# Optimization experiments

Measured on AMD Instinct MI355X. Metric: run time of the kernel, lower is better.

The kernel has to match this reference:

```python
import jax, jax.numpy as jnp
import numpy as np


def setup_inputs() -> dict:
    key = jax.random.key(0)
    ks = jax.random.split(key, 6)
    T, n_vars, n_channels, hidden = 2048, 64, 256, 512
    # VarianceScaling(2.0,'fan_in','uniform') ~ uniform(-limit, limit), limit=sqrt(3*2/fan_in)
    limit = float(np.sqrt(3.0 * 2.0 / n_channels))
    return {
        "enriched_history": jax.random.normal(ks[0], (T, n_vars, n_channels), dtype=jnp.float32),
        "target_mask": jax.random.randint(ks[1], (n_vars,), 0, 2, dtype=jnp.int32),
        "intervention_mask": jax.random.randint(ks[2], (n_vars,), 0, 2, dtype=jnp.int32),
        "W_target": jax.random.uniform(ks[3], (n_channels, hidden), jnp.float32, -limit, limit),
        "b_target": jnp.zeros((hidden,), jnp.float32),
        "W_intervention": jax.random.uniform(ks[4], (n_channels, hidden), jnp.float32, -limit, limit),
        "b_intervention": jnp.zeros((hidden,), jnp.float32),
        "W_other": jax.random.uniform(ks[5], (n_channels, hidden), jnp.float32, -limit, limit),
        "b_other": jnp.zeros((hidden,), jnp.float32),
    }


def reference(enriched_history, target_mask, intervention_mask,
              W_target, b_target, W_intervention, b_intervention,
              W_other, b_other):
    T, n_vars, n_channels = enriched_history.shape
    tm = target_mask.astype(jnp.float32)                       # [n_vars]
    im = intervention_mask.astype(jnp.float32) * (1.0 - tm)    # exclusivity
    om = (1.0 - tm) * (1.0 - im)

    flat = enriched_history.reshape(T * n_vars, n_channels)    # [T*n_vars, C]
    proj_t = flat @ W_target + b_target                        # [T*n_vars, H]
    proj_i = flat @ W_intervention + b_intervention
    proj_o = flat @ W_other + b_other

    # Faithful to original: jnp.repeat(mask, T) -> each variable's flag repeated T times
    tm_flat = jnp.repeat(tm, T)
    im_flat = jnp.repeat(im, T)
    om_flat = jnp.repeat(om, T)

    combined = (proj_t * tm_flat[:, None]
                + proj_i * im_flat[:, None]
                + proj_o * om_flat[:, None])
    return combined.reshape(T, n_vars, -1)
```

## Files before the change

### kernel.cpp

```cpp
#include <hip/hip_runtime.h>

typedef float f32x4 __attribute__((ext_vector_type(4)));
typedef unsigned short u16x8 __attribute__((ext_vector_type(8)));
typedef __bf16 bf16x8 __attribute__((ext_vector_type(8)));

__global__ __launch_bounds__(256) void convert_w_kernel(
    const float* __restrict__ Wt_, const float* __restrict__ Wi_,
    const float* __restrict__ Wo_, unsigned short* __restrict__ out)
{
    __shared__ unsigned short tile[64][72];

    const int b    = blockIdx.x;
    const int role = b >> 5;
    const int kt   = (b & 31) >> 3;
    const int nt   = b & 7;
    const float* __restrict__ W = (role == 0) ? Wt_ : ((role == 1) ? Wi_ : Wo_);

    const int t  = threadIdx.x;
    const int r0 = t >> 4;
    const int c4 = (t & 15) << 2;

#pragma unroll
    for (int j = 0; j < 4; ++j) {
        const int kl = r0 + j * 16;
        f32x4 v = *(const f32x4*)(W + (size_t)(kt * 64 + kl) * 512 + nt * 64 + c4);
#pragma unroll
        for (int e = 0; e < 4; ++e)
            tile[c4 + e][kl] = __builtin_bit_cast(unsigned short, (__bf16)v[e]);
    }
    __syncthreads();

    const int cs = t & 7;
#pragma unroll
    for (int p = 0; p < 2; ++p) {
        const int r = (t >> 3) + p * 32;
        u16x8 v = *(const u16x8*)&tile[r][cs * 8];
        *(u16x8*)(out + (size_t)role * 512 * 256 +
                  (size_t)(nt * 64 + r) * 256 + kt * 64 + cs * 8) = v;
    }
}

__global__ __launch_bounds__(512, 3) void role_proj_kernel(
    const float* __restrict__ A,
    const int* __restrict__ tmask,
    const int* __restrict__ imask,
    const unsigned short* __restrict__ Wws,
    const float* __restrict__ bt, const float* __restrict__ bi,
    const float* __restrict__ bo,
    float* __restrict__ C)
{
    __shared__ unsigned short As[64 * 256];

    const int tid = threadIdx.x;
    const int m0  = blockIdx.x * 64;

    const int mi   = blockIdx.x >> 5;
    const int role = tmask[mi] ? 0 : (imask[mi] ? 1 : 2);
    const unsigned short* __restrict__ W = Wws + (size_t)role * (512 * 256);
    const float* __restrict__ bias = (role == 0) ? bt : ((role == 1) ? bi : bo);

    f32x4 ld[4][2];
#pragma unroll
    for (int j = 0; j < 4; ++j) {
        const int u   = tid + 512 * j;
        const int row = u >> 5;
        const int sl  = u & 31;
        const f32x4* src = (const f32x4*)(A + (size_t)(m0 + row) * 256 + sl * 8);
        ld[j][0] = __builtin_nontemporal_load(src);
        ld[j][1] = __builtin_nontemporal_load(src + 1);
    }
#pragma unroll
    for (int j = 0; j < 4; ++j) {
        const int u   = tid + 512 * j;
        const int row = u >> 5;
        const int sl  = u & 31;
        bf16x8 pk;
        pk[0] = (__bf16)ld[j][0][0]; pk[1] = (__bf16)ld[j][0][1];
        pk[2] = (__bf16)ld[j][0][2]; pk[3] = (__bf16)ld[j][0][3];
        pk[4] = (__bf16)ld[j][1][0]; pk[5] = (__bf16)ld[j][1][1];
        pk[6] = (__bf16)ld[j][1][2]; pk[7] = (__bf16)ld[j][1][3];
        *(bf16x8*)&As[row * 256 + ((sl ^ (row & 7)) << 3)] = pk;
    }
    __syncthreads();

    const int lane  = tid & 63;
    const int wid   = tid >> 6;
    const int l15   = lane & 15;
    const int l4    = lane >> 4;
    const int nbase = wid * 64;
    const int r7    = l15 & 7;

#pragma unroll
    for (int fn = 0; fn < 4; ++fn) {
        const unsigned short* wp =
            W + (size_t)(nbase + fn * 16 + l15) * 256 + l4 * 8;

        f32x4 acc[4] = {};

#pragma unroll 1
        for (int ks = 0; ks < 8; ++ks) {
            const u16x8 bfr = *(const u16x8*)(wp + ks * 32);
            u16x8 afr[4];
#pragma unroll
            for (int fm = 0; fm < 4; ++fm) {
                const int row  = fm * 16 + l15;
                const int slot = (ks * 4 + l4) ^ r7;
                afr[fm] = *(const u16x8*)&As[row * 256 + slot * 8];
            }
#pragma unroll
            for (int fm = 0; fm < 4; ++fm) {
                acc[fm] = __builtin_amdgcn_mfma_f32_16x16x32_bf16(
                    __builtin_bit_cast(bf16x8, bfr),
                    __builtin_bit_cast(bf16x8, afr[fm]),
                    acc[fm], 0, 0, 0);
            }
        }

        const int col = nbase + fn * 16 + l4 * 4;
        const f32x4 bv = *(const f32x4*)(bias + col);
#pragma unroll
        for (int fm = 0; fm < 4; ++fm) {
            const int row = m0 + fm * 16 + l15;
            *(f32x4*)(C + (size_t)row * 512 + col) = acc[fm] + bv;
        }
    }
}

extern "C" void kernel_launch(void* const* d_in, const int* in_sizes, int n_in,
                              void* d_out, int out_size, void* d_ws, size_t ws_size,
                              hipStream_t stream) {
    const float* A   = (const float*)d_in[0];
    const int*   tm  = (const int*)d_in[1];
    const int*   im  = (const int*)d_in[2];
    const float* Wt_ = (const float*)d_in[3];
    const float* bt  = (const float*)d_in[4];
    const float* Wi_ = (const float*)d_in[5];
    const float* bi  = (const float*)d_in[6];
    const float* Wo_ = (const float*)d_in[7];
    const float* bo  = (const float*)d_in[8];

    unsigned short* Wws = (unsigned short*)d_ws;

    hipLaunchKernelGGL(convert_w_kernel, dim3(96), dim3(256),
                       0, stream, Wt_, Wi_, Wo_, Wws);

    hipLaunchKernelGGL(role_proj_kernel, dim3(2048), dim3(512),
                       0, stream, A, tm, im, Wws, bt, bi, bo, (float*)d_out);
}
```

Baseline: 137.4 us.

## Keep A fragments in registers per wave and drop LDS staging

The GEMM kernel no longer stages the A tile in shared memory. Each wave now loads its own 32 rows directly from global memory, converts them to bf16 and keeps them in registers, then loops over all 512 output columns, streaming W fragments from global or L2. This removes LDS writes and reads and the block barrier, and switches to 256-thread blocks with a smaller grid. In exchange each wave reads far more W per MFMA (the whole of W per 32 rows instead of per 64 rows), register pressure rises, and A loads become strided by row instead of fully coalesced.

```diff
diff --git a/kernel.cpp b/kernel.cpp
--- a/kernel.cpp
+++ b/kernel.cpp
@@ -40,7 +40,7 @@
     }
 }
 
-__global__ __launch_bounds__(512, 3) void role_proj_kernel(
+__global__ __launch_bounds__(256, 4) void role_proj_kernel(
     const float* __restrict__ A,
     const int* __restrict__ tmask,
     const int* __restrict__ imask,
@@ -49,80 +49,63 @@
     const float* __restrict__ bo,
     float* __restrict__ C)
 {
-    __shared__ unsigned short As[64 * 256];
+    const int tid  = threadIdx.x;
+    const int lane = tid & 63;
+    const int wid  = tid >> 6;
+    const int l15  = lane & 15;
+    const int l4   = lane >> 4;
 
-    const int tid = threadIdx.x;
-    const int m0  = blockIdx.x * 64;
-
-    const int mi   = blockIdx.x >> 5;
+    const int m0w  = blockIdx.x * 128 + wid * 32;
+    const int mi   = blockIdx.x >> 4;
     const int role = tmask[mi] ? 0 : (imask[mi] ? 1 : 2);
     const unsigned short* __restrict__ W = Wws + (size_t)role * (512 * 256);
     const float* __restrict__ bias = (role == 0) ? bt : ((role == 1) ? bi : bo);
 
-    f32x4 ld[4][2];
+    const float* a0 = A + (size_t)(m0w + l15) * 256 + l4 * 8;
+    const float* a1 = a0 + 16 * 256;
+
+    bf16x8 abf[2][8];
 #pragma unroll
-    for (int j = 0; j < 4; ++j) {
-        const int u   = tid + 512 * j;
-        const int row = u >> 5;
-        const int sl  = u & 31;
-        const f32x4* src = (const f32x4*)(A + (size_t)(m0 + row) * 256 + sl * 8);
-        ld[j][0] = __builtin_nontemporal_load(src);
-        ld[j][1] = __builtin_nontemporal_load(src + 1);
+    for (int ks = 0; ks < 8; ++ks) {
+        f32x4 t00 = *(const f32x4*)(a0 + ks * 32);
+        f32x4 t01 = *(const f32x4*)(a0 + ks * 32 + 4);
+        f32x4 t10 = *(const f32x4*)(a1 + ks * 32);
+        f32x4 t11 = *(const f32x4*)(a1 + ks * 32 + 4);
+        bf16x8 p0 = { (__bf16)t00[0], (__bf16)t00[1], (__bf16)t00[2], (__bf16)t00[3],
+                      (__bf16)t01[0], (__bf16)t01[1], (__bf16)t01[2], (__bf16)t01[3] };
+        bf16x8 p1 = { (__bf16)t10[0], (__bf16)t10[1], (__bf16)t10[2], (__bf16)t10[3],
+                      (__bf16)t11[0], (__bf16)t11[1], (__bf16)t11[2], (__bf16)t11[3] };
+        abf[0][ks] = p0;
+        abf[1][ks] = p1;
     }
-#pragma unroll
-    for (int j = 0; j < 4; ++j) {
-        const int u   = tid + 512 * j;
-        const int row = u >> 5;
-        const int sl  = u & 31;
-        bf16x8 pk;
-        pk[0] = (__bf16)ld[j][0][0]; pk[1] = (__bf16)ld[j][0][1];
-        pk[2] = (__bf16)ld[j][0][2]; pk[3] = (__bf16)ld[j][0][3];
-        pk[4] = (__bf16)ld[j][1][0]; pk[5] = (__bf16)ld[j][1][1];
-        pk[6] = (__bf16)ld[j][1][2]; pk[7] = (__bf16)ld[j][1][3];
-        *(bf16x8*)&As[row * 256 + ((sl ^ (row & 7)) << 3)] = pk;
-    }
-    __syncthreads();
 
-    const int lane  = tid & 63;
-    const int wid   = tid >> 6;
-    const int l15   = lane & 15;
-    const int l4    = lane >> 4;
-    const int nbase = wid * 64;
-    const int r7    = l15 & 7;
-
-#pragma unroll
-    for (int fn = 0; fn < 4; ++fn) {
-        const unsigned short* wp =
-            W + (size_t)(nbase + fn * 16 + l15) * 256 + l4 * 8;
-
-        f32x4 acc[4] = {};
+    const size_t crow0 = (size_t)(m0w + l15) * 512;
+    const size_t crow1 = crow0 + (size_t)16 * 512;
 
 #pragma unroll 1
+    for (int fn = 0; fn < 32; ++fn) {
+        const unsigned short* wp =
+            W + (size_t)(fn * 16 + l15) * 256 + l4 * 8;
+
+        u16x8 bfr[8];
+#pragma unroll
+        for (int ks = 0; ks < 8; ++ks)
+            bfr[ks] = *(const u16x8*)(wp + ks * 32);
+
+        f32x4 acc0 = {};
+        f32x4 acc1 = {};
+#pragma unroll
         for (int ks = 0; ks < 8; ++ks) {
-            const u16x8 bfr = *(const u16x8*)(wp + ks * 32);
-            u16x8 afr[4];
-#pragma unroll
-            for (int fm = 0; fm < 4; ++fm) {
-                const int row  = fm * 16 + l15;
-                const int slot = (ks * 4 + l4) ^ r7;
-                afr[fm] = *(const u16x8*)&As[row * 256 + slot * 8];
-            }
-#pragma unroll
-            for (int fm = 0; fm < 4; ++fm) {
-                acc[fm] = __builtin_amdgcn_mfma_f32_16x16x32_bf16(
-                    __builtin_bit_cast(bf16x8, bfr),
-                    __builtin_bit_cast(bf16x8, afr[fm]),
-                    acc[fm], 0, 0, 0);
-            }
+            acc0 = __builtin_amdgcn_mfma_f32_16x16x32_bf16(
+                __builtin_bit_cast(bf16x8, bfr[ks]), abf[0][ks], acc0, 0, 0, 0);
+            acc1 = __builtin_amdgcn_mfma_f32_16x16x32_bf16(
+                __builtin_bit_cast(bf16x8, bfr[ks]), abf[1][ks], acc1, 0, 0, 0);
         }
 
-        const int col = nbase + fn * 16 + l4 * 4;
+        const int col = fn * 16 + l4 * 4;
         const f32x4 bv = *(const f32x4*)(bias + col);
-#pragma unroll
-        for (int fm = 0; fm < 4; ++fm) {
-            const int row = m0 + fm * 16 + l15;
-            *(f32x4*)(C + (size_t)row * 512 + col) = acc[fm] + bv;
-        }
+        *(f32x4*)(C + crow0 + col) = acc0 + bv;
+        *(f32x4*)(C + crow1 + col) = acc1 + bv;
     }
 }
 
@@ -144,6 +127,6 @@
     hipLaunchKernelGGL(convert_w_kernel, dim3(96), dim3(256),
                        0, stream, Wt_, Wi_, Wo_, Wws);
 
-    hipLaunchKernelGGL(role_proj_kernel, dim3(2048), dim3(512),
+    hipLaunchKernelGGL(role_proj_kernel, dim3(1024), dim3(256),
                        0, stream, A, tm, im, Wws, bt, bi, bo, (float*)d_out);
 }
```

Result: slower. 184.3 us (+34.1%).
